# Optimization experiments

Measured on AMD Instinct MI355X. Metric: run time of the kernel, lower is better.

Reference implementation:

```python
import jax, jax.numpy as jnp
import numpy as np

B, S, E, H = 8, 1024, 768, 12
D = E // H  # per-head dim


def setup_inputs() -> dict:
    key = jax.random.key(0)
    ks = jax.random.split(key, 9)
    glorot = lambda k: jax.random.normal(k, (E, E), jnp.float32) * np.sqrt(2.0 / (E + E))
    return {
        "inputs": jax.random.normal(ks[0], (B, S, E), jnp.float32),
        "Wq": glorot(ks[1]), "bq": jnp.zeros((E,), jnp.float32),
        "Wk": glorot(ks[2]), "bk": jnp.zeros((E,), jnp.float32),
        "Wv": glorot(ks[3]), "bv": jnp.zeros((E,), jnp.float32),
        "Wo": glorot(ks[4]), "bo": jnp.zeros((E,), jnp.float32),
    }


def reference(inputs, Wq, bq, Wk, bk, Wv, bv, Wo, bo):
    b, s, e = inputs.shape
    # QKV projections then split heads: [B,S,E] -> [B,H,S,D]
    def heads(x):
        return x.reshape(b, s, H, D).transpose(0, 2, 1, 3)
    q = heads(inputs @ Wq + bq)
    k = heads(inputs @ Wk + bk)
    v = heads(inputs @ Wv + bv)
    scale = 1.0 / jnp.sqrt(jnp.asarray(D, inputs.dtype))
    scores = jnp.einsum("bhqd,bhkd->bhqk", q, k) * scale
    weights = jax.nn.softmax(scores, axis=-1)  # attn_drop rate 0 -> identity
    attn = jnp.einsum("bhqk,bhkd->bhqd", weights, v)
    concat = attn.transpose(0, 2, 1, 3).reshape(b, s, e)
    out = concat @ Wo + bo  # proj_drop rate 0 -> identity
    return out
```

## Files before the change

kernel.cpp:

```cpp
#include <hip/hip_runtime.h>
#include <math.h>

#define BB 8
#define SS 1024
#define EE 768
#define HH 12
#define DD 64
#define MM (BB*SS)

typedef __attribute__((ext_vector_type(8))) short short8;
typedef __attribute__((ext_vector_type(4))) short short4v;
typedef __attribute__((ext_vector_type(4))) float f32x4;

static __device__ __forceinline__ short f2bf(float x) {
    unsigned u = __float_as_uint(x);
    u += 0x7fffu + ((u >> 16) & 1u);
    return (short)(u >> 16);
}
static __device__ __forceinline__ short f2bf_fast(float x) {
    return (short)((__float_as_uint(x) + 0x8000u) >> 16);
}

static __device__ __forceinline__ void gload_lds16(const void* g, void* l) {
    __builtin_amdgcn_global_load_lds((__attribute__((address_space(1))) void*)g,
                                     (__attribute__((address_space(3))) void*)l,
                                     16, 0, 0);
}

__global__ __launch_bounds__(256)
void cast_x(const float* __restrict__ src, short* __restrict__ dst) {
    const long i = ((long)blockIdx.x * 256 + threadIdx.x) * 4;
    float4 v = *(const float4*)&src[i];
    short4v o;
    o.x = f2bf(v.x); o.y = f2bf(v.y); o.z = f2bf(v.z); o.w = f2bf(v.w);
    *(short4v*)&dst[i] = o;
}

__global__ __launch_bounds__(256)
void wcast_t(const float* __restrict__ W0, const float* __restrict__ W1,
             const float* __restrict__ W2, const float* __restrict__ W3,
             short* __restrict__ Wt) {
    __shared__ short T[64][72];
    const int z = blockIdx.z;
    const float* sp = (z == 0) ? W0 : (z == 1) ? W1 : (z == 2) ? W2 : W3;
    short* dp = Wt + (long)z * EE * EE;
    const int i0 = blockIdx.y * 64;
    const int j0 = blockIdx.x * 64;
    const int tid = threadIdx.x;
#pragma unroll
    for (int rep = 0; rep < 4; ++rep) {
        const int r = (tid >> 4) + rep * 16;
        const int c = (tid & 15) * 4;
        float4 v = *(const float4*)&sp[(long)(i0 + r) * EE + j0 + c];
        T[c + 0][r] = f2bf(v.x);
        T[c + 1][r] = f2bf(v.y);
        T[c + 2][r] = f2bf(v.z);
        T[c + 3][r] = f2bf(v.w);
    }
    __syncthreads();
#pragma unroll
    for (int rep = 0; rep < 4; ++rep) {
        const int rr = (tid >> 4) + rep * 16;
        const int cc = (tid & 15) * 4;
        short4v o;
        o.x = T[rr][cc + 0]; o.y = T[rr][cc + 1];
        o.z = T[rr][cc + 2]; o.w = T[rr][cc + 3];
        *(short4v*)&dp[(long)(j0 + rr) * EE + i0 + cc] = o;
    }
}

#define GEMM_CORE(Abase, Bbase, row0, col0)                                     \
    f32x4 acc[4][4];                                                            \
    _Pragma("unroll") for (int i = 0; i < 4; ++i)                               \
        _Pragma("unroll") for (int j = 0; j < 4; ++j)                           \
            acc[i][j] = (f32x4){0.f, 0.f, 0.f, 0.f};                            \
    const int rm = (w & 1) * 64, cn = (w >> 1) * 64;                            \
    for (int k0 = 0; k0 < EE; k0 += 64) {                                       \
        __syncthreads();                                                        \
        _Pragma("unroll") for (int i = 0; i < 4; ++i) {                         \
            const int chunk = w * 256 + i * 64 + lane;                          \
            const int r = chunk >> 3, c = (chunk & 7) * 8;                      \
            short* ldsA = Al + (w * 256 + i * 64) * 8;                          \
            short* ldsB = Bl + (w * 256 + i * 64) * 8;                          \
            gload_lds16(&Abase[(long)(row0 + r) * EE + k0 + c], ldsA);          \
            gload_lds16(&Bbase[(long)(col0 + r) * EE + k0 + c], ldsB);          \
        }                                                                       \
        __syncthreads();                                                        \
        _Pragma("unroll") for (int ks = 0; ks < 2; ++ks) {                      \
            short8 af[4], bf[4];                                                \
            _Pragma("unroll") for (int t = 0; t < 4; ++t)                       \
                af[t] = *(const short8*)&Al[(rm + t * 16 + m) * 64 + ks * 32 + quad * 8]; \
            _Pragma("unroll") for (int t = 0; t < 4; ++t)                       \
                bf[t] = *(const short8*)&Bl[(cn + t * 16 + m) * 64 + ks * 32 + quad * 8]; \
            _Pragma("unroll") for (int mt = 0; mt < 4; ++mt)                    \
                _Pragma("unroll") for (int nt = 0; nt < 4; ++nt)                \
                    acc[mt][nt] = __builtin_amdgcn_mfma_f32_16x16x32_bf16(      \
                        af[mt], bf[nt], acc[mt][nt], 0, 0, 0);                  \
        }                                                                       \
    }

#define TSTRIDE 134

#define QSCALE 0.1803368801111204f

__global__ __launch_bounds__(256)
void gemm_qkv(const short* __restrict__ Xb, const short* __restrict__ Wt,
              const float* __restrict__ bq, const float* __restrict__ bk,
              const float* __restrict__ bv,
              short* __restrict__ Qb, short* __restrict__ Kb,
              short* __restrict__ Vb) {
    __shared__ short SMEM[128 * TSTRIDE];
    short* const Al = SMEM;
    short* const Bl = SMEM + 128 * 64;
    const int tid = threadIdx.x, w = tid >> 6, lane = tid & 63;
    const int m = lane & 15, quad = lane >> 4;
    const int wsel = blockIdx.x / 6;
    const int colt = blockIdx.x % 6;
    const int row0 = blockIdx.y * 128;
    const int col0 = colt * 128;
    const short* Wsel = Wt + (long)wsel * EE * EE;
    const float* bias = (wsel == 0) ? bq : (wsel == 1) ? bk : bv;

    GEMM_CORE(Xb, Wsel, row0, col0)

    __syncthreads();
    const int b = row0 >> 10, s0 = row0 & 1023;

    if (wsel < 2) {
        const float scale = (wsel == 0) ? QSCALE : 1.0f;
        short* QK = (wsel == 0) ? Qb : Kb;
#pragma unroll
        for (int nt = 0; nt < 4; ++nt) {
            const float bvv = bias[col0 + cn + nt * 16 + m];
#pragma unroll
            for (int mt = 0; mt < 4; ++mt)
#pragma unroll
                for (int r = 0; r < 4; ++r)
                    SMEM[(rm + mt * 16 + quad * 4 + r) * TSTRIDE + cn + nt * 16 + m] =
                        f2bf((acc[mt][nt][r] + bvv) * scale);
        }
        __syncthreads();
#pragma unroll
        for (int rep = 0; rep < 8; ++rep) {
            const int chunk = tid + rep * 256;
            const int row = chunk >> 4;
            const int cc = (chunk & 15) * 8;
            const int colg = col0 + cc;
            const int h = colg >> 6, d = colg & 63;
            short8 v = *(const short8*)&SMEM[row * TSTRIDE + cc];
            *(short8*)&QK[((long)(b * HH + h) * SS + s0 + row) * DD + d] = v;
        }
    } else {
#pragma unroll
        for (int nt = 0; nt < 4; ++nt) {
            const float bvv = bias[col0 + cn + nt * 16 + m];
#pragma unroll
            for (int mt = 0; mt < 4; ++mt) {
                const int rowb = rm + mt * 16 + quad * 4;
                short4v o;
                o.x = f2bf(acc[mt][nt][0] + bvv);
                o.y = f2bf(acc[mt][nt][1] + bvv);
                o.z = f2bf(acc[mt][nt][2] + bvv);
                o.w = f2bf(acc[mt][nt][3] + bvv);
                *(short4v*)&SMEM[(cn + nt * 16 + m) * TSTRIDE + rowb] = o;
            }
        }
        __syncthreads();
#pragma unroll
        for (int rep = 0; rep < 8; ++rep) {
            const int chunk = tid + rep * 256;
            const int col = chunk >> 4;
            const int sc8 = (chunk & 15) * 8;
            const int colg = col0 + col;
            const int h = colg >> 6, d = colg & 63;
            short8 v = *(const short8*)&SMEM[col * TSTRIDE + sc8];
            *(short8*)&Vb[((long)(b * HH + h) * DD + d) * SS + s0 + sc8] = v;
        }
    }
}

__global__ __launch_bounds__(256)
void gemm_proj(const short* __restrict__ Cb, const short* __restrict__ WoT,
               const float* __restrict__ bo, float* __restrict__ out) {
    __shared__ short Al[128 * 64];
    __shared__ short Bl[128 * 64];
    const int tid = threadIdx.x, w = tid >> 6, lane = tid & 63;
    const int m = lane & 15, quad = lane >> 4;
    const int row0 = blockIdx.y * 128;
    const int col0 = blockIdx.x * 128;

    GEMM_CORE(Cb, WoT, row0, col0)

#pragma unroll
    for (int nt = 0; nt < 4; ++nt) {
        const int colg = col0 + cn + nt * 16 + m;
        const float bvv = bo[colg];
#pragma unroll
        for (int mt = 0; mt < 4; ++mt)
#pragma unroll
            for (int r = 0; r < 4; ++r) {
                const int srow = row0 + rm + mt * 16 + quad * 4 + r;
                out[(long)srow * EE + colg] = acc[mt][nt][r] + bvv;
            }
    }
}

__global__ __launch_bounds__(256)
void attn_mfma(const short* __restrict__ Q,
               const short* __restrict__ K,
               const short* __restrict__ Vt,
               short* __restrict__ out) {
    __shared__ short Kl[64 * 72];
    __shared__ short Vl[64 * 72];
    __shared__ short Pl[4 * 32 * 72];

    const int tid  = threadIdx.x;
    const int w    = tid >> 6;
    const int l    = tid & 63;
    const int m    = l & 15;
    const int quad = l >> 4;
    const int h = blockIdx.y, b = blockIdx.z;
    const int q0 = blockIdx.x * 128;
    const long bh = (long)(b * HH + h);

    const short* Qg = Q  + bh * SS * DD;
    const short* Kg = K  + bh * SS * DD;
    const short* Vg = Vt + bh * DD * SS;

    short8 aq[2][2];
#pragma unroll
    for (int g = 0; g < 2; ++g) {
        const int row = q0 + w * 32 + g * 16 + m;
        aq[g][0] = *(const short8*)(Qg + (long)row * DD + quad * 8);
        aq[g][1] = *(const short8*)(Qg + (long)row * DD + 32 + quad * 8);
    }

    short8 ones;
#pragma unroll
    for (int i = 0; i < 8; ++i) ones[i] = (short)0x3F80;

    f32x4 O[2][4], lacc[2];
#pragma unroll
    for (int g = 0; g < 2; ++g) {
        lacc[g] = (f32x4){0.f, 0.f, 0.f, 0.f};
#pragma unroll
        for (int dt = 0; dt < 4; ++dt) O[g][dt] = (f32x4){0.f, 0.f, 0.f, 0.f};
    }

    for (int kt = 0; kt < 16; ++kt) {
        const int k0 = kt * 64;
        __syncthreads();
#pragma unroll
        for (int rep = 0; rep < 2; ++rep) {
            const int seg = tid + rep * 256;
            const int r = seg >> 3, s = seg & 7;
            *(short8*)(Kl + r * 72 + s * 8) =
                *(const short8*)(Kg + (long)(k0 + r) * DD + s * 8);
            *(short8*)(Vl + r * 72 + s * 8) =
                *(const short8*)(Vg + (long)r * SS + k0 + s * 8);
        }
        __syncthreads();

        f32x4 sc[2][4];
#pragma unroll
        for (int nt = 0; nt < 4; ++nt) {
            const short* kb = Kl + (nt * 16 + m) * 72 + quad * 8;
            short8 b0 = *(const short8*)kb;
            short8 b1 = *(const short8*)(kb + 32);
#pragma unroll
            for (int g = 0; g < 2; ++g) {
                f32x4 a = (f32x4){0.f, 0.f, 0.f, 0.f};
                a = __builtin_amdgcn_mfma_f32_16x16x32_bf16(aq[g][0], b0, a, 0, 0, 0);
                a = __builtin_amdgcn_mfma_f32_16x16x32_bf16(aq[g][1], b1, a, 0, 0, 0);
                sc[g][nt] = a;
            }
        }

#pragma unroll
        for (int g = 0; g < 2; ++g)
#pragma unroll
            for (int nt = 0; nt < 4; ++nt)
#pragma unroll
                for (int r = 0; r < 4; ++r)
                    sc[g][nt][r] = __builtin_amdgcn_exp2f(sc[g][nt][r]);

        short* Pw = Pl + w * 32 * 72;
#pragma unroll
        for (int g = 0; g < 2; ++g)
#pragma unroll
            for (int nt = 0; nt < 4; ++nt)
#pragma unroll
                for (int r = 0; r < 4; ++r)
                    Pw[(g * 16 + quad * 4 + r) * 72 + nt * 16 + m] =
                        f2bf_fast(sc[g][nt][r]);

        short8 ap[2][2];
#pragma unroll
        for (int g = 0; g < 2; ++g) {
            ap[g][0] = *(const short8*)(Pw + (g * 16 + m) * 72 + quad * 8);
            ap[g][1] = *(const short8*)(Pw + (g * 16 + m) * 72 + 32 + quad * 8);
        }

#pragma unroll
        for (int g = 0; g < 2; ++g) {
            lacc[g] = __builtin_amdgcn_mfma_f32_16x16x32_bf16(ap[g][0], ones, lacc[g], 0, 0, 0);
            lacc[g] = __builtin_amdgcn_mfma_f32_16x16x32_bf16(ap[g][1], ones, lacc[g], 0, 0, 0);
        }
#pragma unroll
        for (int dt = 0; dt < 4; ++dt) {
            const short* vb = Vl + (dt * 16 + m) * 72 + quad * 8;
            short8 b0 = *(const short8*)vb;
            short8 b1 = *(const short8*)(vb + 32);
#pragma unroll
            for (int g = 0; g < 2; ++g) {
                O[g][dt] = __builtin_amdgcn_mfma_f32_16x16x32_bf16(ap[g][0], b0, O[g][dt], 0, 0, 0);
                O[g][dt] = __builtin_amdgcn_mfma_f32_16x16x32_bf16(ap[g][1], b1, O[g][dt], 0, 0, 0);
            }
        }
    }

#pragma unroll
    for (int g = 0; g < 2; ++g)
#pragma unroll
        for (int r = 0; r < 4; ++r) {
            const float inv = 1.0f / lacc[g][r];
            const int qo = q0 + w * 32 + g * 16 + quad * 4 + r;
            short* orow = out + ((long)(b * SS + qo)) * EE + h * DD;
#pragma unroll
            for (int dt = 0; dt < 4; ++dt)
                orow[dt * 16 + m] = f2bf(O[g][dt][r] * inv);
        }
}

extern "C" void kernel_launch(void* const* d_in, const int* in_sizes, int n_in,
                              void* d_out, int out_size, void* d_ws, size_t ws_size,
                              hipStream_t stream) {
    const float* X  = (const float*)d_in[0];
    const float* Wq = (const float*)d_in[1];
    const float* bq = (const float*)d_in[2];
    const float* Wk = (const float*)d_in[3];
    const float* bk = (const float*)d_in[4];
    const float* Wv = (const float*)d_in[5];
    const float* bv = (const float*)d_in[6];
    const float* Wo = (const float*)d_in[7];
    const float* bo = (const float*)d_in[8];

    const long SEG = (long)BB * HH * SS * DD;
    const long WSEG = (long)EE * EE;
    short* Xb = (short*)d_ws;
    short* Wt = Xb + SEG;
    short* Qb = Wt + 4 * WSEG;
    short* Kb = Qb + SEG;
    short* Vb = Kb + SEG;
    short* Cb = Vb + SEG;

    cast_x<<<dim3(MM * EE / 4 / 256), 256, 0, stream>>>(X, Xb);
    wcast_t<<<dim3(12, 12, 4), 256, 0, stream>>>(Wq, Wk, Wv, Wo, Wt);

    gemm_qkv<<<dim3(18, 64), 256, 0, stream>>>(Xb, Wt, bq, bk, bv, Qb, Kb, Vb);

    attn_mfma<<<dim3(SS / 128, HH, BB), 256, 0, stream>>>(Qb, Kb, Vb, Cb);

    gemm_proj<<<dim3(6, 64), 256, 0, stream>>>(Cb, Wt + 3 * WSEG, bo,
                                               (float*)d_out);
}
```

Baseline: 227.8 us.

## Swap MFMA operand order so accumulators hold contiguous columns for vectorized stores

```diff
diff --git a/kernel.cpp b/kernel.cpp
--- a/kernel.cpp
+++ b/kernel.cpp
@@ -69,7 +69,7 @@
     }
 }
 
-#define GEMM_CORE(Abase, Bbase, row0, col0)                                     \
+#define GEMM_CORE(Abase, Bbase, row0, col0, SWAP)                               \
     f32x4 acc[4][4];                                                            \
     _Pragma("unroll") for (int i = 0; i < 4; ++i)                               \
         _Pragma("unroll") for (int j = 0; j < 4; ++j)                           \
@@ -94,12 +94,15 @@
                 bf[t] = *(const short8*)&Bl[(cn + t * 16 + m) * 64 + ks * 32 + quad * 8]; \
             _Pragma("unroll") for (int mt = 0; mt < 4; ++mt)                    \
                 _Pragma("unroll") for (int nt = 0; nt < 4; ++nt)                \
-                    acc[mt][nt] = __builtin_amdgcn_mfma_f32_16x16x32_bf16(      \
-                        af[mt], bf[nt], acc[mt][nt], 0, 0, 0);                  \
+                    acc[mt][nt] = (SWAP)                                        \
+                        ? __builtin_amdgcn_mfma_f32_16x16x32_bf16(              \
+                              bf[nt], af[mt], acc[mt][nt], 0, 0, 0)             \
+                        : __builtin_amdgcn_mfma_f32_16x16x32_bf16(              \
+                              af[mt], bf[nt], acc[mt][nt], 0, 0, 0);            \
         }                                                                       \
     }
 
-#define TSTRIDE 134
+#define TS 140
 
 #define QSCALE 0.1803368801111204f
 
@@ -109,7 +112,7 @@
               const float* __restrict__ bv,
               short* __restrict__ Qb, short* __restrict__ Kb,
               short* __restrict__ Vb) {
-    __shared__ short SMEM[128 * TSTRIDE];
+    __shared__ short SMEM[128 * TS];
     short* const Al = SMEM;
     short* const Bl = SMEM + 128 * 64;
     const int tid = threadIdx.x, w = tid >> 6, lane = tid & 63;
@@ -119,25 +122,26 @@
     const int row0 = blockIdx.y * 128;
     const int col0 = colt * 128;
     const short* Wsel = Wt + (long)wsel * EE * EE;
-    const float* bias = (wsel == 0) ? bq : (wsel == 1) ? bk : bv;
-
-    GEMM_CORE(Xb, Wsel, row0, col0)
-
-    __syncthreads();
     const int b = row0 >> 10, s0 = row0 & 1023;
 
     if (wsel < 2) {
+        const float* bias = (wsel == 0) ? bq : bk;
+        GEMM_CORE(Xb, Wsel, row0, col0, 1)
+        __syncthreads();
         const float scale = (wsel == 0) ? QSCALE : 1.0f;
         short* QK = (wsel == 0) ? Qb : Kb;
 #pragma unroll
         for (int nt = 0; nt < 4; ++nt) {
-            const float bvv = bias[col0 + cn + nt * 16 + m];
-#pragma unroll
-            for (int mt = 0; mt < 4; ++mt)
-#pragma unroll
-                for (int r = 0; r < 4; ++r)
-                    SMEM[(rm + mt * 16 + quad * 4 + r) * TSTRIDE + cn + nt * 16 + m] =
-                        f2bf((acc[mt][nt][r] + bvv) * scale);
+            float4 b4 = *(const float4*)&bias[col0 + cn + nt * 16 + quad * 4];
+#pragma unroll
+            for (int mt = 0; mt < 4; ++mt) {
+                short4v o;
+                o.x = f2bf((acc[mt][nt][0] + b4.x) * scale);
+                o.y = f2bf((acc[mt][nt][1] + b4.y) * scale);
+                o.z = f2bf((acc[mt][nt][2] + b4.z) * scale);
+                o.w = f2bf((acc[mt][nt][3] + b4.w) * scale);
+                *(short4v*)&SMEM[(rm + mt * 16 + m) * TS + cn + nt * 16 + quad * 4] = o;
+            }
         }
         __syncthreads();
 #pragma unroll
@@ -147,13 +151,15 @@
             const int cc = (chunk & 15) * 8;
             const int colg = col0 + cc;
             const int h = colg >> 6, d = colg & 63;
-            short8 v = *(const short8*)&SMEM[row * TSTRIDE + cc];
+            short8 v = *(const short8*)&SMEM[row * TS + cc];
             *(short8*)&QK[((long)(b * HH + h) * SS + s0 + row) * DD + d] = v;
         }
     } else {
+        GEMM_CORE(Xb, Wsel, row0, col0, 0)
+        __syncthreads();
 #pragma unroll
         for (int nt = 0; nt < 4; ++nt) {
-            const float bvv = bias[col0 + cn + nt * 16 + m];
+            const float bvv = bv[col0 + cn + nt * 16 + m];
 #pragma unroll
             for (int mt = 0; mt < 4; ++mt) {
                 const int rowb = rm + mt * 16 + quad * 4;
@@ -162,7 +168,7 @@
                 o.y = f2bf(acc[mt][nt][1] + bvv);
                 o.z = f2bf(acc[mt][nt][2] + bvv);
                 o.w = f2bf(acc[mt][nt][3] + bvv);
-                *(short4v*)&SMEM[(cn + nt * 16 + m) * TSTRIDE + rowb] = o;
+                *(short4v*)&SMEM[(cn + nt * 16 + m) * TS + rowb] = o;
             }
         }
         __syncthreads();
@@ -173,7 +179,7 @@
             const int sc8 = (chunk & 15) * 8;
             const int colg = col0 + col;
             const int h = colg >> 6, d = colg & 63;
-            short8 v = *(const short8*)&SMEM[col * TSTRIDE + sc8];
+            short8 v = *(const short8*)&SMEM[col * TS + sc8];
             *(short8*)&Vb[((long)(b * HH + h) * DD + d) * SS + s0 + sc8] = v;
         }
     }
@@ -189,21 +195,26 @@
     const int row0 = blockIdx.y * 128;
     const int col0 = blockIdx.x * 128;
 
-    GEMM_CORE(Cb, WoT, row0, col0)
+    GEMM_CORE(Cb, WoT, row0, col0, 1)
 
 #pragma unroll
     for (int nt = 0; nt < 4; ++nt) {
-        const int colg = col0 + cn + nt * 16 + m;
-        const float bvv = bo[colg];
-#pragma unroll
-        for (int mt = 0; mt < 4; ++mt)
-#pragma unroll
-            for (int r = 0; r < 4; ++r) {
-                const int srow = row0 + rm + mt * 16 + quad * 4 + r;
-                out[(long)srow * EE + colg] = acc[mt][nt][r] + bvv;
-            }
-    }
-}
+        const int colg = col0 + cn + nt * 16 + quad * 4;
+        float4 b4 = *(const float4*)&bo[colg];
+#pragma unroll
+        for (int mt = 0; mt < 4; ++mt) {
+            const int srow = row0 + rm + mt * 16 + m;
+            float4 v;
+            v.x = acc[mt][nt][0] + b4.x;
+            v.y = acc[mt][nt][1] + b4.y;
+            v.z = acc[mt][nt][2] + b4.z;
+            v.w = acc[mt][nt][3] + b4.w;
+            *(float4*)&out[(long)srow * EE + colg] = v;
+        }
+    }
+}
+
+#define PTS 76
 
 __global__ __launch_bounds__(256)
 void attn_mfma(const short* __restrict__ Q,
@@ -212,7 +223,7 @@
                short* __restrict__ out) {
     __shared__ short Kl[64 * 72];
     __shared__ short Vl[64 * 72];
-    __shared__ short Pl[4 * 32 * 72];
+    __shared__ short Pl[4 * 32 * PTS];
 
     const int tid  = threadIdx.x;
     const int w    = tid >> 6;
@@ -239,10 +250,10 @@
 #pragma unroll
     for (int i = 0; i < 8; ++i) ones[i] = (short)0x3F80;
 
-    f32x4 O[2][4], lacc[2];
+    f32x4 O[2][4], lT[2];
 #pragma unroll
     for (int g = 0; g < 2; ++g) {
-        lacc[g] = (f32x4){0.f, 0.f, 0.f, 0.f};
+        lT[g] = (f32x4){0.f, 0.f, 0.f, 0.f};
 #pragma unroll
         for (int dt = 0; dt < 4; ++dt) O[g][dt] = (f32x4){0.f, 0.f, 0.f, 0.f};
     }
@@ -265,71 +276,70 @@
 #pragma unroll
         for (int nt = 0; nt < 4; ++nt) {
             const short* kb = Kl + (nt * 16 + m) * 72 + quad * 8;
-            short8 b0 = *(const short8*)kb;
-            short8 b1 = *(const short8*)(kb + 32);
+            short8 k0f = *(const short8*)kb;
+            short8 k1f = *(const short8*)(kb + 32);
 #pragma unroll
             for (int g = 0; g < 2; ++g) {
                 f32x4 a = (f32x4){0.f, 0.f, 0.f, 0.f};
-                a = __builtin_amdgcn_mfma_f32_16x16x32_bf16(aq[g][0], b0, a, 0, 0, 0);
-                a = __builtin_amdgcn_mfma_f32_16x16x32_bf16(aq[g][1], b1, a, 0, 0, 0);
+                a = __builtin_amdgcn_mfma_f32_16x16x32_bf16(k0f, aq[g][0], a, 0, 0, 0);
+                a = __builtin_amdgcn_mfma_f32_16x16x32_bf16(k1f, aq[g][1], a, 0, 0, 0);
                 sc[g][nt] = a;
             }
         }
 
+        short* Pw = Pl + w * 32 * PTS;
 #pragma unroll
         for (int g = 0; g < 2; ++g)
 #pragma unroll
-            for (int nt = 0; nt < 4; ++nt)
-#pragma unroll
-                for (int r = 0; r < 4; ++r)
-                    sc[g][nt][r] = __builtin_amdgcn_exp2f(sc[g][nt][r]);
-
-        short* Pw = Pl + w * 32 * 72;
-#pragma unroll
-        for (int g = 0; g < 2; ++g)
-#pragma unroll
-            for (int nt = 0; nt < 4; ++nt)
-#pragma unroll
-                for (int r = 0; r < 4; ++r)
-                    Pw[(g * 16 + quad * 4 + r) * 72 + nt * 16 + m] =
-                        f2bf_fast(sc[g][nt][r]);
+            for (int nt = 0; nt < 4; ++nt) {
+                short4v p;
+                p.x = f2bf_fast(__builtin_amdgcn_exp2f(sc[g][nt][0]));
+                p.y = f2bf_fast(__builtin_amdgcn_exp2f(sc[g][nt][1]));
+                p.z = f2bf_fast(__builtin_amdgcn_exp2f(sc[g][nt][2]));
+                p.w = f2bf_fast(__builtin_amdgcn_exp2f(sc[g][nt][3]));
+                *(short4v*)&Pw[(g * 16 + m) * PTS + nt * 16 + quad * 4] = p;
+            }
 
         short8 ap[2][2];
 #pragma unroll
         for (int g = 0; g < 2; ++g) {
-            ap[g][0] = *(const short8*)(Pw + (g * 16 + m) * 72 + quad * 8);
-            ap[g][1] = *(const short8*)(Pw + (g * 16 + m) * 72 + 32 + quad * 8);
+            ap[g][0] = *(const short8*)&Pw[(g * 16 + m) * PTS + quad * 8];
+            ap[g][1] = *(const short8*)&Pw[(g * 16 + m) * PTS + 32 + quad * 8];
         }
 
 #pragma unroll
         for (int g = 0; g < 2; ++g) {
-            lacc[g] = __builtin_amdgcn_mfma_f32_16x16x32_bf16(ap[g][0], ones, lacc[g], 0, 0, 0);
-            lacc[g] = __builtin_amdgcn_mfma_f32_16x16x32_bf16(ap[g][1], ones, lacc[g], 0, 0, 0);
+            lT[g] = __builtin_amdgcn_mfma_f32_16x16x32_bf16(ones, ap[g][0], lT[g], 0, 0, 0);
+            lT[g] = __builtin_amdgcn_mfma_f32_16x16x32_bf16(ones, ap[g][1], lT[g], 0, 0, 0);
         }
 #pragma unroll
         for (int dt = 0; dt < 4; ++dt) {
             const short* vb = Vl + (dt * 16 + m) * 72 + quad * 8;
-            short8 b0 = *(const short8*)vb;
-            short8 b1 = *(const short8*)(vb + 32);
+            short8 v0 = *(const short8*)vb;
+            short8 v1 = *(const short8*)(vb + 32);
 #pragma unroll
             for (int g = 0; g < 2; ++g) {
-                O[g][dt] = __builtin_amdgcn_mfma_f32_16x16x32_bf16(ap[g][0], b0, O[g][dt], 0, 0, 0);
-                O[g][dt] = __builtin_amdgcn_mfma_f32_16x16x32_bf16(ap[g][1], b1, O[g][dt], 0, 0, 0);
-            }
-        }
-    }
-
-#pragma unroll
-    for (int g = 0; g < 2; ++g)
-#pragma unroll
-        for (int r = 0; r < 4; ++r) {
-            const float inv = 1.0f / lacc[g][r];
-            const int qo = q0 + w * 32 + g * 16 + quad * 4 + r;
-            short* orow = out + ((long)(b * SS + qo)) * EE + h * DD;
-#pragma unroll
-            for (int dt = 0; dt < 4; ++dt)
-                orow[dt * 16 + m] = f2bf(O[g][dt][r] * inv);
-        }
+                O[g][dt] = __builtin_amdgcn_mfma_f32_16x16x32_bf16(v0, ap[g][0], O[g][dt], 0, 0, 0);
+                O[g][dt] = __builtin_amdgcn_mfma_f32_16x16x32_bf16(v1, ap[g][1], O[g][dt], 0, 0, 0);
+            }
+        }
+    }
+
+#pragma unroll
+    for (int g = 0; g < 2; ++g) {
+        const float inv = 1.0f / lT[g][0];
+        const int qo = q0 + w * 32 + g * 16 + m;
+        short* orow = out + ((long)(b * SS + qo)) * EE + h * DD;
+#pragma unroll
+        for (int dt = 0; dt < 4; ++dt) {
+            short4v o;
+            o.x = f2bf(O[g][dt][0] * inv);
+            o.y = f2bf(O[g][dt][1] * inv);
+            o.z = f2bf(O[g][dt][2] * inv);
+            o.w = f2bf(O[g][dt][3] * inv);
+            *(short4v*)&orow[dt * 16 + quad * 4] = o;
+        }
+    }
 }
 
 extern "C" void kernel_launch(void* const* d_in, const int* in_sizes, int n_in,
```

Measured after the change: 242.0 us. 1.06x slower.
